# Optimization experiments

Measured on AMD Instinct MI355X. Metric: run time of the kernel, lower is better.

The kernel has to match this reference:

```python
import jax, jax.numpy as jnp
import numpy as np

NUM_CLUSTERS = 64
DIM = 256
EPS = 1e-12  # torch F.normalize eps


def setup_inputs() -> dict:
    key = jax.random.key(0)
    k1, k2, k3, k4 = jax.random.split(key, 4)
    x = jax.random.normal(k1, (128, DIM, 32, 32), dtype=jnp.float32)
    # nn.Conv2d(256, K, 1) params: weight (K, C, 1, 1) -> store as (K, C); bias (K,)
    fan_in = DIM
    bound = 1.0 / np.sqrt(fan_in)
    conv_w = jax.random.uniform(k2, (NUM_CLUSTERS, DIM), jnp.float32, -bound, bound)
    conv_b = jax.random.uniform(k3, (NUM_CLUSTERS,), jnp.float32, -bound, bound)
    centroids = jax.random.uniform(k4, (NUM_CLUSTERS, DIM), jnp.float32)  # torch.rand
    return {"x": x, "conv_w": conv_w, "conv_b": conv_b, "centroids": centroids}


def _l2norm(v, axis):
    n = jnp.sqrt(jnp.sum(v * v, axis=axis, keepdims=True))
    return v / jnp.maximum(n, EPS)


def reference(x, conv_w, conv_b, centroids):
    N, C, H, W = x.shape
    K = conv_w.shape[0]
    # L2-normalize over channel dim
    x = _l2norm(x, axis=1)                      # (N, C, H, W)
    xf = x.reshape(N, C, H * W)                 # (N, C, P)
    # 1x1 conv == per-pixel linear over channels
    logits = jnp.einsum('ncp,kc->nkp', xf, conv_w) + conv_b[None, :, None]
    a = jax.nn.softmax(logits, axis=1)          # (N, K, P) softmax over clusters
    # VLAD via matmul decomposition: sum_p a[n,k,p]*(x[n,:,p] - c[k,:])
    agg = jnp.einsum('nkp,ncp->nkc', a, xf)     # (N, K, C)
    asum = jnp.sum(a, axis=-1)                  # (N, K)
    vlad = agg - asum[:, :, None] * centroids[None, :, :]
    vlad = _l2norm(vlad, axis=2)                # intra-normalization
    vlad = vlad.reshape(N, K * C)
    return _l2norm(vlad, axis=1)
```

## Files before the change

kernel.cpp:

```cpp
#include <hip/hip_runtime.h>
#include <math.h>


#define EPSF 1e-12f

typedef __attribute__((ext_vector_type(8))) __bf16 bf16x8;
typedef __attribute__((ext_vector_type(4))) float f32x4;
typedef __attribute__((ext_vector_type(4))) unsigned int u32x4;

#define MFMA(a, b, c) __builtin_amdgcn_mfma_f32_16x16x32_bf16((a), (b), (c), 0, 0, 0)

__device__ __forceinline__ bf16x8 as_bf(u32x4 v) { return __builtin_bit_cast(bf16x8, v); }

__device__ __forceinline__ unsigned packsplit(float x) {
    const unsigned u  = __float_as_uint(x);
    const unsigned hi = u & 0xFFFF0000u;
    const float lof   = x - __uint_as_float(hi);
    return hi | (__float_as_uint(lof) >> 16);
}

struct u32pair { unsigned h, l; };

__device__ __forceinline__ u32pair splitpair(float f0, float f1) {
    const unsigned u0 = __float_as_uint(f0), u1 = __float_as_uint(f1);
    u32pair r;
    r.h = __builtin_amdgcn_perm(u1, u0, 0x07060302u);
    const float l0 = f0 - __uint_as_float(u0 & 0xFFFF0000u);
    const float l1 = f1 - __uint_as_float(u1 & 0xFFFF0000u);
    r.l = __builtin_amdgcn_perm(__float_as_uint(l1), __float_as_uint(l0), 0x07060302u);
    return r;
}

__device__ __forceinline__ void unpack2q(const u32x4 q0, const u32x4 q1,
                                         u32x4& hi, u32x4& lo) {
    hi[0] = __builtin_amdgcn_perm(q0[1], q0[0], 0x07060302u);
    lo[0] = __builtin_amdgcn_perm(q0[1], q0[0], 0x05040100u);
    hi[1] = __builtin_amdgcn_perm(q0[3], q0[2], 0x07060302u);
    lo[1] = __builtin_amdgcn_perm(q0[3], q0[2], 0x05040100u);
    hi[2] = __builtin_amdgcn_perm(q1[1], q1[0], 0x07060302u);
    lo[2] = __builtin_amdgcn_perm(q1[1], q1[0], 0x05040100u);
    hi[3] = __builtin_amdgcn_perm(q1[3], q1[2], 0x07060302u);
    lo[3] = __builtin_amdgcn_perm(q1[3], q1[2], 0x05040100u);
}

__device__ __forceinline__ void split8v(const float* xv, u32x4& hi, u32x4& lo) {
    #pragma unroll
    for (int w2 = 0; w2 < 4; ++w2) {
        const u32pair r = splitpair(xv[2*w2], xv[2*w2+1]);
        hi[w2] = r.h;
        lo[w2] = r.l;
    }
}

__global__ void split_w_kernel(const float* __restrict__ wmat,
                               unsigned* __restrict__ whiG,
                               unsigned* __restrict__ wloG) {
    const int idx = blockIdx.x * 256 + threadIdx.x;
    const int mt = idx >> 9, s = (idx >> 6) & 7, l = idx & 63;
    const int k = mt * 16 + (l & 15);
    const int cb = s * 32 + 8 * (l >> 4);
    const float* wr = wmat + k * 256 + cb;
    const float4 f0 = *(const float4*)wr;
    const float4 f1 = *(const float4*)(wr + 4);
    const float xv[8] = {f0.x, f0.y, f0.z, f0.w, f1.x, f1.y, f1.z, f1.w};
    u32x4 hi, lo; split8v(xv, hi, lo);
    *(u32x4*)(whiG + idx * 4) = hi;
    *(u32x4*)(wloG + idx * 4) = lo;
}

__global__ __launch_bounds__(256, 3) void netvlad_mfma(
    const float* __restrict__ x,
    const unsigned* __restrict__ whiG, const unsigned* __restrict__ wloG,
    const float* __restrict__ bias, float* __restrict__ out,
    float* __restrict__ asum_g) {

    __shared__ __align__(16) unsigned smem[10240];
    __shared__ __align__(16) float rn_lds[128];
    __shared__ __align__(16) float sspart[256];
    unsigned* const p1hi = smem;
    unsigned* const p1lo = smem + 5120;
    unsigned* const abuf = smem;
    unsigned* const p2hi = smem;
    unsigned* const p2lo = smem + 4352;

    const int t = threadIdx.x;
    const int w = t >> 6, l = t & 63;
    const int l15 = l & 15, lg4 = l >> 4;
    const int n = blockIdx.x >> 3, e = blockIdx.x & 7;
    const size_t ximg = (size_t)n * 256 * 1024;
    const int p0 = e * 128;
    const int k0 = w * 16;
    const int cs = lg4 * 8;

    const int pp = t & 127, half = t >> 7;
    const float* xg1 = x + ximg + (size_t)(half * 16) * 1024 + p0 + pp;
    unsigned* const w1hi = p1hi + pp * 20 + half * 8;
    unsigned* const w1lo = p1lo + pp * 20 + half * 8;
    float g[16];
    float ssacc = 0.f;

    #define P1_LOAD(s_) { _Pragma("unroll")                                   \
        for (int i = 0; i < 16; ++i)                                          \
            g[i] = xg1[(size_t)((s_) * 32 + i) * 1024]; }
    #define P1_WRITE(b_) {                                                    \
        u32x4 vh0, vl0, vh1, vl1;                                             \
        _Pragma("unroll")                                                     \
        for (int j = 0; j < 4; ++j) {                                         \
            const u32pair r0 = splitpair(g[2*j],   g[2*j+1]);                 \
            const u32pair r1 = splitpair(g[8+2*j], g[8+2*j+1]);               \
            vh0[j] = r0.h; vl0[j] = r0.l;                                     \
            vh1[j] = r1.h; vl1[j] = r1.l;                                     \
        }                                                                     \
        _Pragma("unroll")                                                     \
        for (int i = 0; i < 16; ++i) ssacc = fmaf(g[i], g[i], ssacc);         \
        *(u32x4*)(w1hi + (b_) * 2560)     = vh0;                              \
        *(u32x4*)(w1hi + (b_) * 2560 + 4) = vh1;                              \
        *(u32x4*)(w1lo + (b_) * 2560)     = vl0;                              \
        *(u32x4*)(w1lo + (b_) * 2560 + 4) = vl1; }

    f32x4 acc1[4][2];
    #pragma unroll
    for (int i = 0; i < 4; ++i) {
        acc1[i][0] = f32x4{0.f, 0.f, 0.f, 0.f};
        acc1[i][1] = f32x4{0.f, 0.f, 0.f, 0.f};
    }

    P1_LOAD(0);
    P1_WRITE(0);
    #pragma unroll
    for (int s = 0; s < 8; ++s) {
        if (s < 7) P1_LOAD(s + 1);
        __syncthreads();
        const unsigned* shi = p1hi + (s & 1) * 2560;
        const unsigned* slo = p1lo + (s & 1) * 2560;
        u32x4 wh[4], wl[4];
        #pragma unroll
        for (int mt = 0; mt < 4; ++mt) {
            const int fo = ((mt * 8 + s) * 64 + l) * 4;
            wh[mt] = *(const u32x4*)(whiG + fo);
            wl[mt] = *(const u32x4*)(wloG + fo);
        }
        u32x4 bhi[2], blo[2];
        #pragma unroll
        for (int ntl = 0; ntl < 2; ++ntl) {
            const int ro = ((2 * w + ntl) * 16 + l15) * 20 + lg4 * 4;
            bhi[ntl] = *(const u32x4*)(shi + ro);
            blo[ntl] = *(const u32x4*)(slo + ro);
        }
        #pragma unroll
        for (int mt = 0; mt < 4; ++mt) {
            #pragma unroll
            for (int ntl = 0; ntl < 2; ++ntl) {
                acc1[mt][ntl] = MFMA(as_bf(wh[mt]), as_bf(bhi[ntl]), acc1[mt][ntl]);
                acc1[mt][ntl] = MFMA(as_bf(wh[mt]), as_bf(blo[ntl]), acc1[mt][ntl]);
                acc1[mt][ntl] = MFMA(as_bf(wl[mt]), as_bf(bhi[ntl]), acc1[mt][ntl]);
            }
        }
        if (s < 7) P1_WRITE((s + 1) & 1);
    }
    sspart[t] = ssacc;

    f32x4 biasv[4];
    #pragma unroll
    for (int mt = 0; mt < 4; ++mt)
        biasv[mt] = *(const f32x4*)(bias + mt * 16 + 4 * lg4);

    const int r2 = t >> 4;
    const int pq8 = (t & 15) * 8;
    const float* xg2 = x + ximg + (size_t)r2 * 1024 + p0 + pq8;
    unsigned* const w2hi = p2hi + r2 * 68 + (pq8 >> 1);
    unsigned* const w2lo = p2lo + r2 * 68 + (pq8 >> 1);
    float4 g2[4];
    #define P2_LOAD(s_) { _Pragma("unroll")                                   \
        for (int i = 0; i < 2; ++i) {                                         \
            g2[i*2]   = *(const float4*)(xg2 + (size_t)((s_)*32 + 16*i)*1024);    \
            g2[i*2+1] = *(const float4*)(xg2 + (size_t)((s_)*32 + 16*i)*1024 + 4);\
        } }
    #define P2_WRITE(b_) { _Pragma("unroll")                                  \
        for (int i = 0; i < 2; ++i) {                                         \
            u32x4 vh, vl;                                                     \
            const u32pair ra = splitpair(g2[i*2].x,   g2[i*2].y);             \
            const u32pair rb = splitpair(g2[i*2].z,   g2[i*2].w);             \
            const u32pair rc = splitpair(g2[i*2+1].x, g2[i*2+1].y);           \
            const u32pair rd = splitpair(g2[i*2+1].z, g2[i*2+1].w);           \
            vh[0] = ra.h; vl[0] = ra.l;                                       \
            vh[1] = rb.h; vl[1] = rb.l;                                       \
            vh[2] = rc.h; vl[2] = rc.l;                                       \
            vh[3] = rd.h; vl[3] = rd.l;                                       \
            *(u32x4*)(w2hi + (b_) * 2176 + i * 1088) = vh;                    \
            *(u32x4*)(w2lo + (b_) * 2176 + i * 1088) = vl; } }
    P2_LOAD(0);
    __syncthreads();

    if (t < 128)
        rn_lds[t] = 1.f / fmaxf(sqrtf(sspart[t] + sspart[t + 128]), EPSF);
    __syncthreads();

    #pragma unroll
    for (int ntl = 0; ntl < 2; ++ntl) {
        const int p = (2 * w + ntl) * 16 + l15;
        const float rn = rn_lds[p];
        float lgv[16];
        #pragma unroll
        for (int mt = 0; mt < 4; ++mt)
            #pragma unroll
            for (int r = 0; r < 4; ++r)
                lgv[mt * 4 + r] = fmaf(acc1[mt][ntl][r], rn, biasv[mt][r]);
        float mx = lgv[0];
        #pragma unroll
        for (int i = 1; i < 16; ++i) mx = fmaxf(mx, lgv[i]);
        mx = fmaxf(mx, __shfl_xor(mx, 16));
        mx = fmaxf(mx, __shfl_xor(mx, 32));
        float den = 0.f;
        #pragma unroll
        for (int i = 0; i < 16; ++i) { lgv[i] = __expf(lgv[i] - mx); den += lgv[i]; }
        den += __shfl_xor(den, 16);
        den += __shfl_xor(den, 32);
        const float inv = 1.f / den;
        #pragma unroll
        for (int mt = 0; mt < 4; ++mt)
            #pragma unroll
            for (int r = 0; r < 4; ++r)
                abuf[(mt * 16 + 4 * lg4 + r) * 132 + p] =
                    packsplit(lgv[mt * 4 + r] * inv);
    }
    __syncthreads();

    u32x4 aphi[4], aplo[4];
    f32x4 asum_acc = f32x4{0.f, 0.f, 0.f, 0.f};
    const u32x4 ONES = {0x3F803F80u, 0x3F803F80u, 0x3F803F80u, 0x3F803F80u};
    #pragma unroll
    for (int ks = 0; ks < 4; ++ks) {
        const unsigned* ap = abuf + (k0 + l15) * 132 + ks * 32 + cs;
        const u32x4 pa = *(const u32x4*)ap;
        const u32x4 pb = *(const u32x4*)(ap + 4);
        u32x4 ahi, alo; unpack2q(pa, pb, ahi, alo);
        asum_acc = MFMA(as_bf(ahi), as_bf(ONES), asum_acc);
        asum_acc = MFMA(as_bf(alo), as_bf(ONES), asum_acc);
        const float* rp = rn_lds + ks * 32 + cs;
        const unsigned paw[8] = {pa[0],pa[1],pa[2],pa[3],pb[0],pb[1],pb[2],pb[3]};
        float av[8];
        #pragma unroll
        for (int j = 0; j < 8; ++j) {
            const float afv = __uint_as_float(paw[j] & 0xFFFF0000u)
                            + __uint_as_float(paw[j] << 16);
            av[j] = afv * rp[j];
        }
        split8v(av, aphi[ks], aplo[ks]);
    }
    __syncthreads();

    P2_WRITE(0);

    float* op = out + (size_t)n * 16384;
    #pragma unroll
    for (int s2 = 0; s2 < 8; ++s2) {
        if (s2 < 7) P2_LOAD(s2 + 1);
        __syncthreads();
        const unsigned* shi = p2hi + (s2 & 1) * 2176;
        const unsigned* slo = p2lo + (s2 & 1) * 2176;
        f32x4 a2[2];
        #pragma unroll
        for (int ntl = 0; ntl < 2; ++ntl) {
            a2[ntl] = f32x4{0.f, 0.f, 0.f, 0.f};
            #pragma unroll
            for (int ks = 0; ks < 4; ++ks) {
                const int ro = (ntl * 16 + l15) * 68 + ks * 16 + lg4 * 4;
                const u32x4 xhi = *(const u32x4*)(shi + ro);
                const u32x4 xlo = *(const u32x4*)(slo + ro);
                a2[ntl] = MFMA(as_bf(aphi[ks]), as_bf(xhi), a2[ntl]);
                a2[ntl] = MFMA(as_bf(aphi[ks]), as_bf(xlo), a2[ntl]);
                a2[ntl] = MFMA(as_bf(aplo[ks]), as_bf(xhi), a2[ntl]);
            }
        }
        if (s2 < 7) P2_WRITE((s2 + 1) & 1);
        #pragma unroll
        for (int ntl = 0; ntl < 2; ++ntl) {
            const int c = s2 * 32 + ntl * 16 + l15;
            #pragma unroll
            for (int r = 0; r < 4; ++r)
                atomicAdd(&op[(k0 + lg4 * 4 + r) * 256 + c], a2[ntl][r]);
        }
    }
    if (l15 == 0) {
        #pragma unroll
        for (int r = 0; r < 4; ++r)
            atomicAdd(&asum_g[n * 64 + k0 + lg4 * 4 + r], asum_acc[r]);
    }
}

__global__ __launch_bounds__(256) void netvlad_epi(
    float* __restrict__ out, const float* __restrict__ asum_g,
    const float* __restrict__ cent) {
    __shared__ float wred[4];
    __shared__ float gs_sh;
    const int n = blockIdx.x;
    const int t = threadIdx.x;
    const int k = t >> 2;
    const int q = t & 3;
    float* op = out + (size_t)n * 16384 + k * 256 + q * 64;
    const float* cp = cent + k * 256 + q * 64;
    const float as = asum_g[n * 64 + k];

    float v[64];
    float ss = 0.f;
    #pragma unroll
    for (int i = 0; i < 64; i += 4) {
        const float4 av = *(const float4*)&op[i];
        const float4 cv = *(const float4*)&cp[i];
        v[i+0] = fmaf(-as, cv.x, av.x);
        v[i+1] = fmaf(-as, cv.y, av.y);
        v[i+2] = fmaf(-as, cv.z, av.z);
        v[i+3] = fmaf(-as, cv.w, av.w);
        ss = fmaf(v[i+0], v[i+0], ss);
        ss = fmaf(v[i+1], v[i+1], ss);
        ss = fmaf(v[i+2], v[i+2], ss);
        ss = fmaf(v[i+3], v[i+3], ss);
    }
    ss += __shfl_xor(ss, 1);
    ss += __shfl_xor(ss, 2);
    const float iscale = 1.f / fmaxf(sqrtf(ss), EPSF);

    float gsum = (q == 0) ? ss * iscale * iscale : 0.f;
    #pragma unroll
    for (int off = 4; off < 64; off <<= 1) gsum += __shfl_xor(gsum, off);
    if ((t & 63) == 0) wred[t >> 6] = gsum;
    __syncthreads();
    if (t == 0) {
        const float tot = wred[0] + wred[1] + wred[2] + wred[3];
        gs_sh = 1.f / fmaxf(sqrtf(tot), EPSF);
    }
    __syncthreads();
    const float fs = iscale * gs_sh;
    #pragma unroll
    for (int i = 0; i < 64; i += 4) {
        float4 w4;
        w4.x = v[i+0] * fs; w4.y = v[i+1] * fs;
        w4.z = v[i+2] * fs; w4.w = v[i+3] * fs;
        *(float4*)&op[i] = w4;
    }
}

extern "C" void kernel_launch(void* const* d_in, const int* in_sizes, int n_in,
                              void* d_out, int out_size, void* d_ws, size_t ws_size,
                              hipStream_t stream) {
    (void)in_sizes; (void)n_in; (void)ws_size;
    const float* x    = (const float*)d_in[0];
    const float* wmat = (const float*)d_in[1];
    const float* b    = (const float*)d_in[2];
    const float* cent = (const float*)d_in[3];
    float* out = (float*)d_out;
    unsigned* whiG = (unsigned*)d_ws;
    unsigned* wloG = whiG + 8192;
    float* asum_g  = (float*)(whiG + 16384);

    hipMemsetAsync(d_out, 0, (size_t)out_size * sizeof(float), stream);
    hipMemsetAsync(asum_g, 0, 128 * 64 * sizeof(float), stream);
    split_w_kernel<<<8, 256, 0, stream>>>(wmat, whiG, wloG);
    netvlad_mfma<<<1024, 256, 0, stream>>>(x, whiG, wloG, b, out, asum_g);
    netvlad_epi<<<128, 256, 0, stream>>>(out, asum_g, cent);
}
```

Baseline: 101.0 us.

## Deepen phase-1 prefetch, shrink LDS padding, raise occupancy, reorder block mapping

Phase-1 global loads now use two register buffers so loads are issued two stages ahead instead of one, which hides more global latency. The LDS row stride drops from 20 to 18 words to cut shared memory use, and launch bounds rise to 4 blocks per SM. Blocks are remapped so consecutive blocks take different images with the same pixel slice. The per-pixel inverse norm is now computed directly by each lane, removing a separate step and one barrier. The extra register buffer risks spills under the tighter bound, and the new stride may change LDS bank conflicts.

```diff
diff --git a/kernel.cpp b/kernel.cpp
--- a/kernel.cpp
+++ b/kernel.cpp
@@ -68,17 +68,17 @@
     *(u32x4*)(wloG + idx * 4) = lo;
 }
 
-__global__ __launch_bounds__(256, 3) void netvlad_mfma(
+__global__ __launch_bounds__(256, 4) void netvlad_mfma(
     const float* __restrict__ x,
     const unsigned* __restrict__ whiG, const unsigned* __restrict__ wloG,
     const float* __restrict__ bias, float* __restrict__ out,
     float* __restrict__ asum_g) {
 
-    __shared__ __align__(16) unsigned smem[10240];
+    __shared__ __align__(16) unsigned smem[9216];
     __shared__ __align__(16) float rn_lds[128];
     __shared__ __align__(16) float sspart[256];
     unsigned* const p1hi = smem;
-    unsigned* const p1lo = smem + 5120;
+    unsigned* const p1lo = smem + 4608;
     unsigned* const abuf = smem;
     unsigned* const p2hi = smem;
     unsigned* const p2lo = smem + 4352;
@@ -86,7 +86,7 @@
     const int t = threadIdx.x;
     const int w = t >> 6, l = t & 63;
     const int l15 = l & 15, lg4 = l >> 4;
-    const int n = blockIdx.x >> 3, e = blockIdx.x & 7;
+    const int n = blockIdx.x & 127, e = blockIdx.x >> 7;
     const size_t ximg = (size_t)n * 256 * 1024;
     const int p0 = e * 128;
     const int k0 = w * 16;
@@ -94,29 +94,29 @@
 
     const int pp = t & 127, half = t >> 7;
     const float* xg1 = x + ximg + (size_t)(half * 16) * 1024 + p0 + pp;
-    unsigned* const w1hi = p1hi + pp * 20 + half * 8;
-    unsigned* const w1lo = p1lo + pp * 20 + half * 8;
-    float g[16];
+    unsigned* const w1hi = p1hi + pp * 18 + half * 8;
+    unsigned* const w1lo = p1lo + pp * 18 + half * 8;
+    float gA[16], gB[16];
     float ssacc = 0.f;
 
-    #define P1_LOAD(s_) { _Pragma("unroll")                                   \
+    #define P1_LOAD(gv_, s_) { _Pragma("unroll")                              \
         for (int i = 0; i < 16; ++i)                                          \
-            g[i] = xg1[(size_t)((s_) * 32 + i) * 1024]; }
-    #define P1_WRITE(b_) {                                                    \
+            gv_[i] = xg1[(size_t)((s_) * 32 + i) * 1024]; }
+    #define P1_WRITE(gv_, b_) {                                               \
         u32x4 vh0, vl0, vh1, vl1;                                             \
         _Pragma("unroll")                                                     \
         for (int j = 0; j < 4; ++j) {                                         \
-            const u32pair r0 = splitpair(g[2*j],   g[2*j+1]);                 \
-            const u32pair r1 = splitpair(g[8+2*j], g[8+2*j+1]);               \
+            const u32pair r0 = splitpair(gv_[2*j],   gv_[2*j+1]);             \
+            const u32pair r1 = splitpair(gv_[8+2*j], gv_[8+2*j+1]);           \
             vh0[j] = r0.h; vl0[j] = r0.l;                                     \
             vh1[j] = r1.h; vl1[j] = r1.l;                                     \
         }                                                                     \
         _Pragma("unroll")                                                     \
-        for (int i = 0; i < 16; ++i) ssacc = fmaf(g[i], g[i], ssacc);         \
-        *(u32x4*)(w1hi + (b_) * 2560)     = vh0;                              \
-        *(u32x4*)(w1hi + (b_) * 2560 + 4) = vh1;                              \
-        *(u32x4*)(w1lo + (b_) * 2560)     = vl0;                              \
-        *(u32x4*)(w1lo + (b_) * 2560 + 4) = vl1; }
+        for (int i = 0; i < 16; ++i) ssacc = fmaf(gv_[i], gv_[i], ssacc);     \
+        *(u32x4*)(w1hi + (b_) * 2304)     = vh0;                              \
+        *(u32x4*)(w1hi + (b_) * 2304 + 4) = vh1;                              \
+        *(u32x4*)(w1lo + (b_) * 2304)     = vl0;                              \
+        *(u32x4*)(w1lo + (b_) * 2304 + 4) = vl1; }
 
     f32x4 acc1[4][2];
     #pragma unroll
@@ -125,14 +125,18 @@
         acc1[i][1] = f32x4{0.f, 0.f, 0.f, 0.f};
     }
 
-    P1_LOAD(0);
-    P1_WRITE(0);
+    P1_LOAD(gA, 0);
+    P1_LOAD(gB, 1);
+    P1_WRITE(gA, 0);
     #pragma unroll
     for (int s = 0; s < 8; ++s) {
-        if (s < 7) P1_LOAD(s + 1);
+        if (s < 6) {
+            if ((s & 1) == 0) { P1_LOAD(gA, s + 2); }
+            else              { P1_LOAD(gB, s + 2); }
+        }
         __syncthreads();
-        const unsigned* shi = p1hi + (s & 1) * 2560;
-        const unsigned* slo = p1lo + (s & 1) * 2560;
+        const unsigned* shi = p1hi + (s & 1) * 2304;
+        const unsigned* slo = p1lo + (s & 1) * 2304;
         u32x4 wh[4], wl[4];
         #pragma unroll
         for (int mt = 0; mt < 4; ++mt) {
@@ -143,7 +147,7 @@
         u32x4 bhi[2], blo[2];
         #pragma unroll
         for (int ntl = 0; ntl < 2; ++ntl) {
-            const int ro = ((2 * w + ntl) * 16 + l15) * 20 + lg4 * 4;
+            const int ro = ((2 * w + ntl) * 16 + l15) * 18 + lg4 * 4;
             bhi[ntl] = *(const u32x4*)(shi + ro);
             blo[ntl] = *(const u32x4*)(slo + ro);
         }
@@ -156,7 +160,10 @@
                 acc1[mt][ntl] = MFMA(as_bf(wl[mt]), as_bf(bhi[ntl]), acc1[mt][ntl]);
             }
         }
-        if (s < 7) P1_WRITE((s + 1) & 1);
+        if (s < 7) {
+            if ((s & 1) == 0) { P1_WRITE(gB, 1); }
+            else              { P1_WRITE(gA, 0); }
+        }
     }
     sspart[t] = ssacc;
 
@@ -192,14 +199,11 @@
     P2_LOAD(0);
     __syncthreads();
 
-    if (t < 128)
-        rn_lds[t] = 1.f / fmaxf(sqrtf(sspart[t] + sspart[t + 128]), EPSF);
-    __syncthreads();
-
     #pragma unroll
     for (int ntl = 0; ntl < 2; ++ntl) {
         const int p = (2 * w + ntl) * 16 + l15;
-        const float rn = rn_lds[p];
+        const float rn = 1.f / fmaxf(sqrtf(sspart[p] + sspart[p + 128]), EPSF);
+        if (lg4 == 0) rn_lds[p] = rn;
         float lgv[16];
         #pragma unroll
         for (int mt = 0; mt < 4; ++mt)
```

Result: slower. 105.0 us (+4.0%).
